# Performance work log

Measured on AMD Instinct MI355X. Metric: run time of the kernel, lower is better.

## Reference

```python
import jax, jax.numpy as jnp
import numpy as np
from jax import lax

D_MODEL, D_STATE, D_CONV, EXPAND = 64, 16, 4, 2
D_INNER = EXPAND * D_MODEL          # 128
DT_RANK = (D_MODEL + 15) // 16      # 4 = ceil(d_model/16), mamba_ssm 'auto'
B, L, N_IDX = 512, 256, 2048


def setup_inputs() -> dict:
    key = jax.random.key(0)
    ks = jax.random.split(key, 14)
    g = lambda k, shape, s: jax.random.normal(k, shape, jnp.float32) * s
    return {
        "reads": jax.random.normal(ks[0], (B, L, 4), jnp.float32),
        "sequenced_reads_indices": jax.random.randint(ks[1], (N_IDX,), 0, B),
        "exp_w": g(ks[2], (4, D_MODEL), 0.5),
        "exp_b": jnp.zeros((D_MODEL,), jnp.float32),
        "in_proj_w": g(ks[3], (D_MODEL, 2 * D_INNER), 0.1),
        "conv_w": g(ks[4], (D_INNER, 1, D_CONV), 0.3),
        "conv_b": jnp.zeros((D_INNER,), jnp.float32),
        "x_proj_w": g(ks[5], (D_INNER, DT_RANK + 2 * D_STATE), 0.1),
        "dt_w": g(ks[6], (DT_RANK, D_INNER), 0.3),
        "dt_b": jnp.full((D_INNER,), -4.6, jnp.float32),  # softplus(-4.6) ~ 0.01, mamba dt init scale
        "A_log": jnp.log(jnp.broadcast_to(jnp.arange(1, D_STATE + 1, dtype=jnp.float32), (D_INNER, D_STATE))),
        "D_skip": jnp.ones((D_INNER,), jnp.float32),
        "out_proj_w": g(ks[7], (D_INNER, D_MODEL), 0.1),
        "q_w": g(ks[8], (2 * D_MODEL, D_MODEL), 0.1),
        "q_b": jnp.zeros((D_MODEL,), jnp.float32),
        "k_w": g(ks[9], (2 * D_MODEL, D_MODEL), 0.1),
        "k_b": jnp.zeros((D_MODEL,), jnp.float32),
    }


def _mamba(x, in_proj_w, conv_w, conv_b, x_proj_w, dt_w, dt_b, A_log, D_skip, out_proj_w):
    # x: [b, l, d_model]
    xm, z = jnp.split(x @ in_proj_w, 2, axis=-1)  # each [b, l, d_inner]
    # causal depthwise conv over the sequence axis (pad left by d_conv-1, truncate to l)
    xc = lax.conv_general_dilated(
        xm.transpose(0, 2, 1), conv_w, (1,), [(D_CONV - 1, 0)],
        dimension_numbers=("NCH", "OIH", "NCH"), feature_group_count=D_INNER)
    xc = jax.nn.silu(xc + conv_b[None, :, None]).transpose(0, 2, 1)  # [b, l, d_inner]
    dt, Bm, Cm = jnp.split(xc @ x_proj_w, [DT_RANK, DT_RANK + D_STATE], axis=-1)
    delta = jax.nn.softplus(dt @ dt_w + dt_b)  # [b, l, d_inner]
    A = -jnp.exp(A_log)                        # [d_inner, d_state]

    def step(h, inp):
        d_t, B_t, C_t, u_t = inp  # [b,di], [b,ds], [b,ds], [b,di]
        h = jnp.exp(d_t[:, :, None] * A) * h + (d_t * u_t)[:, :, None] * B_t[:, None, :]
        return h, jnp.einsum("bdn,bn->bd", h, C_t)

    h0 = jnp.zeros((x.shape[0], D_INNER, D_STATE), x.dtype)
    xs = (delta.transpose(1, 0, 2), Bm.transpose(1, 0, 2),
          Cm.transpose(1, 0, 2), xc.transpose(1, 0, 2))
    _, ys = lax.scan(jax.checkpoint(step), h0, xs)  # ys: [l, b, d_inner]
    y = ys.transpose(1, 0, 2) + xc * D_skip
    return (y * jax.nn.silu(z)) @ out_proj_w  # [b, l, d_model]


def reference(reads, sequenced_reads_indices, exp_w, exp_b, in_proj_w, conv_w, conv_b,
              x_proj_w, dt_w, dt_b, A_log, D_skip, out_proj_w, q_w, q_b, k_w, k_b):
    x = reads @ exp_w + exp_b  # [b, l, d_model]
    enc = _mamba(x, in_proj_w, conv_w, conv_b, x_proj_w, dt_w, dt_b, A_log, D_skip, out_proj_w)
    mean_pooled = enc.mean(axis=1)        # [b, d_model]
    last_pooled = enc[:, -1, :]           # [b, d_model] (max pool computed in torch but unused)
    pooled = jnp.concatenate([mean_pooled, last_pooled], axis=-1)  # [b, 2*d_model]
    seq = pooled[sequenced_reads_indices]  # [n, 2*d_model]
    queries = seq @ q_w + q_b
    keys = pooled @ k_w + k_b
    return jnp.einsum("nd,md->nm", queries, keys)  # [n, b]
```

## Files before the change

### kernel.cpp

```cpp
#include <hip/hip_runtime.h>
#include <math.h>

#define L_SEQ 256
#define TILE 32
#define NSEG 8

typedef __attribute__((ext_vector_type(2))) float f32x2;
typedef __attribute__((ext_vector_type(4))) float f32x4;
typedef __attribute__((ext_vector_type(8))) _Float16 f16x8;

__device__ __forceinline__ f32x2 fma2(f32x2 a, f32x2 b, f32x2 c) {
    return __builtin_elementwise_fma(a, b, c);
}
__device__ __forceinline__ f32x2 splat2(float x) { f32x2 v = {x, x}; return v; }
__device__ __forceinline__ float silu_f(float x) { return x / (1.f + __expf(-x)); }
__device__ __forceinline__ float sp2_f(float x) {
    return log2f(1.f + exp2f(x * 1.44269504f)) * 0.69314718f;
}

__global__ __launch_bounds__(256)
void k_prep(const float* __restrict__ exp_w, const float* __restrict__ exp_b,
            const float* __restrict__ in_proj_w, const float* __restrict__ x_proj_w,
            const float* __restrict__ dt_w,
            const float* __restrict__ conv_w, const float* __restrict__ conv_b,
            _Float16* __restrict__ WT, _Float16* __restrict__ W2, float* __restrict__ bias2)
{
    const int t = threadIdx.x, blk = blockIdx.x;
    if (blk < 5) {
        const int base = blk * 4096;
        for (int i = base + t; i < base + 4096; i += 256) {
            const int row = i >> 7, k = i & 127;
            float v;
            if (row < 128) {
                v = x_proj_w[k * 36 + 0] * dt_w[row]
                  + x_proj_w[k * 36 + 1] * dt_w[128 + row]
                  + x_proj_w[k * 36 + 2] * dt_w[256 + row]
                  + x_proj_w[k * 36 + 3] * dt_w[384 + row];
            } else {
                v = x_proj_w[k * 36 + 4 + (row - 128)];
            }
            WT[i] = (_Float16)v;
        }
    } else {
        const int d = t & 127;
        const int col = (t < 128) ? d : (128 + d);
        float w0 = 0, w1 = 0, w2 = 0, w3 = 0, bb = 0;
        for (int k = 0; k < 64; ++k) {
            float w = in_proj_w[k * 256 + col];
            w0 = fmaf(exp_w[k], w, w0);
            w1 = fmaf(exp_w[64 + k], w, w1);
            w2 = fmaf(exp_w[128 + k], w, w2);
            w3 = fmaf(exp_w[192 + k], w, w3);
            bb = fmaf(exp_b[k], w, bb);
        }
        const float wx[4] = {w0, w1, w2, w3};
        if (t < 128) {
            for (int j = 0; j < 32; ++j) {
                float v = 0.f;
                if (j < 16)      v = conv_w[d * 4 + (j >> 2)] * wx[j & 3];
                else if (j < 20) v = conv_w[d * 4 + (j - 16)] * bb;
                W2[d * 32 + j] = (_Float16)v;
            }
            bias2[d] = conv_b[d];
        } else {
            for (int j = 0; j < 32; ++j) {
                float v = 0.f;
                if (j >= 12 && j < 16) v = wx[j - 12];
                else if (j == 19)      v = bb;
                W2[(128 + d) * 32 + j] = (_Float16)v;
            }
        }
    }
}

__global__ __launch_bounds__(512, 2)
void mamba_seg2(const float* __restrict__ reads,
                const _Float16* __restrict__ WT, const _Float16* __restrict__ W2,
                const float* __restrict__ bias2, const float* __restrict__ dt_b,
                const float* __restrict__ A_log, const float* __restrict__ D_skip,
                f16x8* __restrict__ QPK, float* __restrict__ GS,
                float* __restrict__ CZ, float* __restrict__ SL, int Bn)
{
    const int bx = blockIdx.x;
    const int b = bx >> 2, jp = bx & 3;
    const int t = threadIdx.x;
    const int lane256 = t & 255, wg = t >> 8;
    const int dd = lane256 >> 1, g = lane256 & 1;
    const int sidx = jp * 2 + wg;

    __shared__ __align__(16) _Float16 F2[2][32 * 40];
    __shared__ __align__(16) _Float16 XC2[2][32 * 136];
    __shared__ __align__(16) float    BC2[2][32 * 32];
    __shared__ _Float16               ZS2[2][32 * 128];
    __shared__ _Float16               DE2[2][32 * 128];

    const float dskip = D_skip[dd];
    const float c1 = -1.44269504f * (float)(8 * g + 1);
    bool structured = true;
#pragma unroll
    for (int k = 0; k < 8; ++k) {
        float a = -__expf(A_log[dd * 16 + g * 8 + k]);
        structured = structured && (fabsf(a + (float)(g * 8 + k + 1)) < 1e-3f);
    }

    for (int i = t; i < 2 * 32 * 40; i += 512) {
        const int tau = i / 1280, r = i - tau * 1280;
        const int l = r / 40, j = r - l * 40;
        const int l_off = jp * 64 + tau * 32;
        _Float16 v = (_Float16)0.f;
        if (j < 16) {
            const int row = l_off + l - 3 + (j >> 2);
            if (row >= 0) v = (_Float16)reads[((size_t)b * L_SEQ + row) * 4 + (j & 3)];
        } else if (j < 20) {
            v = (l_off + l - 3 + (j - 16) >= 0) ? (_Float16)1.f : (_Float16)0.f;
        }
        F2[0][i] = v;
    }
    __syncthreads();

    const int lane = t & 63, wv = t >> 6;
    const int fcol = lane & 15, kq = lane >> 4, rbase = kq * 4;

#pragma unroll
    for (int i = 0; i < 8; ++i) {
        const int tt = wv + 8 * i;
        const int tau = tt >> 5, tid = tt & 31;
        const int m = tid & 1, n = tid >> 1;
        f16x8 af = *(const f16x8*)&F2[tau][(m * 16 + fcol) * 40 + kq * 8];
        f16x8 bf = *(const f16x8*)&W2[(n * 16 + fcol) * 32 + kq * 8];
        f32x4 acc = {0.f, 0.f, 0.f, 0.f};
        acc = __builtin_amdgcn_mfma_f32_16x16x32_f16(af, bf, acc, 0, 0, 0);
        if (n < 8) {
            const int ch = n * 16 + fcol;
            const float bv = bias2[ch];
#pragma unroll
            for (int r = 0; r < 4; ++r)
                XC2[tau][(m * 16 + rbase + r) * 136 + ch] = (_Float16)silu_f(acc[r] + bv);
        } else {
            const int ch = (n - 8) * 16 + fcol;
#pragma unroll
            for (int r = 0; r < 4; ++r)
                ZS2[tau][(m * 16 + rbase + r) * 128 + ch] = (_Float16)silu_f(acc[r]);
        }
    }
    __syncthreads();

#pragma unroll
    for (int i = 0; i < 5; ++i) {
        const int tt = wv + 8 * i;
        const int tau = (tt >= 20) ? 1 : 0, tid = tt - 20 * tau;
        const int m = tid & 1, n = tid >> 1;
        f32x4 acc = {0.f, 0.f, 0.f, 0.f};
#pragma unroll
        for (int ks = 0; ks < 4; ++ks) {
            const int ko = ks * 32 + kq * 8;
            f16x8 af = *(const f16x8*)&XC2[tau][(m * 16 + fcol) * 136 + ko];
            f16x8 bf = *(const f16x8*)&WT[(n * 16 + fcol) * 128 + ko];
            acc = __builtin_amdgcn_mfma_f32_16x16x32_f16(af, bf, acc, 0, 0, 0);
        }
        if (n < 8) {
            const int ch = n * 16 + fcol;
            const float db = dt_b[ch];
#pragma unroll
            for (int r = 0; r < 4; ++r)
                DE2[tau][(m * 16 + rbase + r) * 128 + ch] = (_Float16)sp2_f(acc[r] + db);
        } else {
            const int jb = (n - 8) * 16 + fcol;
#pragma unroll
            for (int r = 0; r < 4; ++r)
                BC2[tau][(m * 16 + rbase + r) * 32 + jb] = acc[r];
        }
    }
    __syncthreads();

    f32x2 h2[4], P2[4], K2[4];
#pragma unroll
    for (int k = 0; k < 4; ++k) { h2[k] = splat2(0.f); P2[k] = splat2(1.f); K2[k] = splat2(0.f); }
    float gsum = 0.f;
    {
        const _Float16* DEw = DE2[wg];
        const _Float16* ZSw = ZS2[wg];
        const _Float16* XCw = XC2[wg];
        const float*    BCw = BC2[wg];
        auto scan_loop = [&](bool needpk) {
            for (int l = 0; l < TILE; ++l) {
                const float de = (float)DEw[l * 128 + dd];
                const float zs = (float)ZSw[l * 128 + dd];
                const float xc = (float)XCw[l * 136 + dd];
                const float du = de * xc;
                f32x2 E2[4];
                if (structured) {
                    const float r = exp2f(de * -1.44269504f);
                    const float t1 = exp2f(de * c1);
                    const float r2 = r * r;
                    E2[0] = (f32x2){t1, t1 * r};
                    const f32x2 r2s = splat2(r2);
                    E2[1] = E2[0] * r2s;
                    E2[2] = E2[1] * r2s;
                    E2[3] = E2[2] * r2s;
                } else {
#pragma unroll
                    for (int k = 0; k < 4; ++k) {
                        float e0 = exp2f(de * (-__expf(A_log[dd * 16 + g * 8 + 2 * k])) * 1.44269504f);
                        float e1 = exp2f(de * (-__expf(A_log[dd * 16 + g * 8 + 2 * k + 1])) * 1.44269504f);
                        E2[k] = (f32x2){e0, e1};
                    }
                }
                const float4 Bq0 = *(const float4*)&BCw[l * 32 + g * 8];
                const float4 Bq1 = *(const float4*)&BCw[l * 32 + g * 8 + 4];
                const float4 Cq0 = *(const float4*)&BCw[l * 32 + 16 + g * 8];
                const float4 Cq1 = *(const float4*)&BCw[l * 32 + 16 + g * 8 + 4];
                const f32x2 B2[4] = {{Bq0.x, Bq0.y}, {Bq0.z, Bq0.w}, {Bq1.x, Bq1.y}, {Bq1.z, Bq1.w}};
                const f32x2 C2[4] = {{Cq0.x, Cq0.y}, {Cq0.z, Cq0.w}, {Cq1.x, Cq1.y}, {Cq1.z, Cq1.w}};
                const f32x2 dus = splat2(du), zss = splat2(zs);
                f32x2 yp2 = splat2(0.f);
#pragma unroll
                for (int k = 0; k < 4; ++k) {
                    h2[k] = fma2(E2[k], h2[k], dus * B2[k]);
                    yp2 = fma2(h2[k], C2[k], yp2);
                    if (needpk) {
                        P2[k] = P2[k] * E2[k];
                        K2[k] = fma2(zss, C2[k] * P2[k], K2[k]);
                    }
                }
                float yp = yp2.x + yp2.y;
                const float y = yp + __shfl_xor(yp, 1);
                gsum += fmaf(xc, dskip, y) * zs;
            }
        };
        if (sidx == 0) scan_loop(false);
        else           scan_loop(true);
    }

    {
        const size_t sb = (size_t)sidx * Bn + b;
#pragma unroll
        for (int k = 0; k < 4; ++k) {
            const int p = g * 4 + k;
            f16x8 v;
            v[0] = (_Float16)h2[k].x; v[1] = (_Float16)h2[k].y;
            v[2] = (_Float16)P2[k].x; v[3] = (_Float16)P2[k].y;
            v[4] = (_Float16)K2[k].x; v[5] = (_Float16)K2[k].y;
            v[6] = (_Float16)0.f;     v[7] = (_Float16)0.f;
            QPK[(sb * 8 + p) * 128 + dd] = v;
        }
        if (g == 0) GS[sb * 128 + dd] = gsum;
        if (jp == 3 && wg == 1) {
            const float zs_last = (float)ZS2[1][(TILE - 1) * 128 + dd];
            const float xc_last = (float)XC2[1][(TILE - 1) * 136 + dd];
#pragma unroll
            for (int k = 0; k < 8; ++k)
                CZ[((size_t)b * 16 + g * 8 + k) * 128 + dd] =
                    zs_last * BC2[1][(TILE - 1) * 32 + 16 + g * 8 + k];
            if (g == 0) SL[(size_t)b * 128 + dd] = zs_last * xc_last * dskip;
        }
    }
}

template<int NS>
__global__ __launch_bounds__(128)
void stitch(const f16x8* __restrict__ QPK, const float* __restrict__ GS,
            const float* __restrict__ CZ, const float* __restrict__ SL,
            const float* __restrict__ out_proj_w,
            const float* __restrict__ k_w, const float* __restrict__ k_b,
            float* __restrict__ pooled, float* __restrict__ keysT, int Bn)
{
    const int b = blockIdx.x, d = threadIdx.x;
    __shared__ float gb[256];
    __shared__ float pl[128];

    float h[16];
    float gsum = GS[(size_t)b * 128 + d];
#pragma unroll
    for (int p = 0; p < 8; ++p) {
        f16x8 v = QPK[((size_t)b * 8 + p) * 128 + d];
        h[2 * p] = (float)v[0]; h[2 * p + 1] = (float)v[1];
    }
#pragma unroll
    for (int s = 1; s < NS; ++s) {
        const size_t sb = (size_t)s * Bn + b;
        gsum += GS[sb * 128 + d];
        float corr = 0.f;
#pragma unroll
        for (int p = 0; p < 8; ++p) {
            f16x8 v = QPK[(sb * 8 + p) * 128 + d];
            corr = fmaf((float)v[4], h[2 * p], corr);
            corr = fmaf((float)v[5], h[2 * p + 1], corr);
            h[2 * p]     = fmaf((float)v[2], h[2 * p],     (float)v[0]);
            h[2 * p + 1] = fmaf((float)v[3], h[2 * p + 1], (float)v[1]);
        }
        gsum += corr;
    }
    float glast = SL[(size_t)b * 128 + d];
#pragma unroll
    for (int n = 0; n < 16; ++n)
        glast = fmaf(CZ[((size_t)b * 16 + n) * 128 + d], h[n], glast);

    gb[d] = gsum * (1.f / (float)L_SEQ);
    gb[128 + d] = glast;
    __syncthreads();
    {
        const int half = d >> 6, oc = d & 63;
        const float* gbp = &gb[half * 128];
        float s = 0.f;
#pragma unroll 16
        for (int i = 0; i < 128; ++i) s = fmaf(gbp[i], out_proj_w[i * 64 + oc], s);
        pooled[(size_t)b * 128 + d] = s;
        pl[d] = s;
    }
    __syncthreads();
    if (d < 64) {
        float s = k_b[d];
#pragma unroll 16
        for (int i = 0; i < 128; ++i) s = fmaf(pl[i], k_w[i * 64 + d], s);
        keysT[(size_t)d * Bn + b] = s;
    }
}

__global__ __launch_bounds__(128)
void qk_kernel(const float* __restrict__ pooled, const int* __restrict__ idx,
               const float* __restrict__ q_w, const float* __restrict__ q_b,
               const float* __restrict__ keysT, float* __restrict__ out, int B, int N)
{
    const int n0 = blockIdx.x * 2, t = threadIdx.x;
    const int n1 = n0 + 1;
    const bool has1 = (n1 < N);
    __shared__ float p0[128], p1[128];
    __shared__ float q0[64], q1[64];
    const int bi0 = idx[n0];
    const int bi1 = has1 ? idx[n1] : bi0;
    p0[t] = pooled[(size_t)bi0 * 128 + t];
    p1[t] = pooled[(size_t)bi1 * 128 + t];
    __syncthreads();
    if (t < 64) {
        float s = q_b[t];
#pragma unroll
        for (int i = 0; i < 128; ++i) s = fmaf(p0[i], q_w[i * 64 + t], s);
        q0[t] = s;
    } else {
        const int tt = t - 64;
        float s = q_b[tt];
#pragma unroll
        for (int i = 0; i < 128; ++i) s = fmaf(p1[i], q_w[i * 64 + tt], s);
        q1[tt] = s;
    }
    __syncthreads();
    for (int m0 = t * 4; m0 < B; m0 += 512) {
        f32x4 a0 = {0.f, 0.f, 0.f, 0.f}, a1 = {0.f, 0.f, 0.f, 0.f};
#pragma unroll 8
        for (int i = 0; i < 64; ++i) {
            const float4 kv = *(const float4*)&keysT[(size_t)i * B + m0];
            const float qa = q0[i], qb = q1[i];
            a0[0] = fmaf(qa, kv.x, a0[0]); a0[1] = fmaf(qa, kv.y, a0[1]);
            a0[2] = fmaf(qa, kv.z, a0[2]); a0[3] = fmaf(qa, kv.w, a0[3]);
            a1[0] = fmaf(qb, kv.x, a1[0]); a1[1] = fmaf(qb, kv.y, a1[1]);
            a1[2] = fmaf(qb, kv.z, a1[2]); a1[3] = fmaf(qb, kv.w, a1[3]);
        }
        *(f32x4*)&out[(size_t)n0 * B + m0] = a0;
        if (has1) *(f32x4*)&out[(size_t)n1 * B + m0] = a1;
    }
}


extern "C" void kernel_launch(void* const* d_in, const int* in_sizes, int n_in,
                              void* d_out, int out_size, void* d_ws, size_t ws_size,
                              hipStream_t stream)
{
    const float* reads      = (const float*)d_in[0];
    const int*   idx        = (const int*)d_in[1];
    const float* exp_w      = (const float*)d_in[2];
    const float* exp_b      = (const float*)d_in[3];
    const float* in_proj_w  = (const float*)d_in[4];
    const float* conv_w     = (const float*)d_in[5];
    const float* conv_b     = (const float*)d_in[6];
    const float* x_proj_w   = (const float*)d_in[7];
    const float* dt_w       = (const float*)d_in[8];
    const float* dt_b       = (const float*)d_in[9];
    const float* A_log      = (const float*)d_in[10];
    const float* D_skip     = (const float*)d_in[11];
    const float* out_proj_w = (const float*)d_in[12];
    const float* q_w        = (const float*)d_in[13];
    const float* q_b        = (const float*)d_in[14];
    const float* k_w        = (const float*)d_in[15];
    const float* k_b        = (const float*)d_in[16];

    const int B = in_sizes[0] / (L_SEQ * 4);
    const int N = in_sizes[1];

    char* wsb = (char*)d_ws;
    size_t off = 0;
    auto alloc = [&](size_t bytes) {
        size_t o = off;
        off = (off + bytes + 255) & ~(size_t)255;
        return o;
    };

    float*     pooled = (float*)(wsb + alloc((size_t)B * 128 * 4));
    float*     keysT  = (float*)(wsb + alloc((size_t)B * 64 * 4));
    _Float16*  WT     = (_Float16*)(wsb + alloc(160 * 128 * 2));
    _Float16*  W2     = (_Float16*)(wsb + alloc(256 * 32 * 2));
    float*     bias2  = (float*)(wsb + alloc(128 * 4));

    const size_t pairs = (size_t)B * NSEG * 8 * 128;
    f16x8* QPK = (f16x8*)(wsb + alloc(pairs * 16));
    float* GS  = (float*)(wsb + alloc((size_t)B * NSEG * 128 * 4));
    float* CZ  = (float*)(wsb + alloc((size_t)B * 16 * 128 * 4));
    float* SL  = (float*)(wsb + alloc((size_t)B * 128 * 4));

    k_prep<<<6, 256, 0, stream>>>(exp_w, exp_b, in_proj_w, x_proj_w, dt_w,
                                  conv_w, conv_b, WT, W2, bias2);
    mamba_seg2<<<B * 4, 512, 0, stream>>>(reads, WT, W2, bias2, dt_b,
                                          A_log, D_skip, QPK, GS, CZ, SL, B);
    stitch<NSEG><<<B, 128, 0, stream>>>(QPK, GS, CZ, SL, out_proj_w, k_w, k_b,
                                        pooled, keysT, B);
    qk_kernel<<<(N + 1) / 2, 128, 0, stream>>>(pooled, idx, q_w, q_b, keysT,
                                               (float*)d_out, B, N);
}
```

Measured before the change: 147.5 us.

## Split scan into 16 segments of 16 steps, split QPK into packed arrays

The chunked Mamba scan now uses 16 segments of 16 timesteps, each handled by its own 256-thread block, instead of 512-thread blocks that each ran two 32-step segments. Shorter serial scans and more independent blocks aim to raise occupancy and cut the sequential latency per block. The padded f16x8 QPK records are replaced by three separate f16x2 arrays, and P/K are skipped for the first segment, which reduces global write and read traffic. In exchange the stitch kernel does twice as many serial combine steps, and the MFMA tiles are half-filled with 16-row tiles.

```diff
diff --git a/kernel.cpp b/kernel.cpp
--- a/kernel.cpp
+++ b/kernel.cpp
@@ -2,12 +2,13 @@
 #include <math.h>
 
 #define L_SEQ 256
-#define TILE 32
-#define NSEG 8
+#define TILE 16
+#define NSEG 16
 
 typedef __attribute__((ext_vector_type(2))) float f32x2;
 typedef __attribute__((ext_vector_type(4))) float f32x4;
 typedef __attribute__((ext_vector_type(8))) _Float16 f16x8;
+typedef __attribute__((ext_vector_type(2))) _Float16 f16x2;
 
 __device__ __forceinline__ f32x2 fma2(f32x2 a, f32x2 b, f32x2 c) {
     return __builtin_elementwise_fma(a, b, c);
@@ -73,26 +74,26 @@
     }
 }
 
-__global__ __launch_bounds__(512, 2)
-void mamba_seg2(const float* __restrict__ reads,
-                const _Float16* __restrict__ WT, const _Float16* __restrict__ W2,
-                const float* __restrict__ bias2, const float* __restrict__ dt_b,
-                const float* __restrict__ A_log, const float* __restrict__ D_skip,
-                f16x8* __restrict__ QPK, float* __restrict__ GS,
-                float* __restrict__ CZ, float* __restrict__ SL, int Bn)
+__global__ __launch_bounds__(256, 6)
+void mamba_seg(const float* __restrict__ reads,
+               const _Float16* __restrict__ WT, const _Float16* __restrict__ W2,
+               const float* __restrict__ bias2, const float* __restrict__ dt_b,
+               const float* __restrict__ A_log, const float* __restrict__ D_skip,
+               f16x2* __restrict__ Qg, f16x2* __restrict__ Pg, f16x2* __restrict__ Kg,
+               float* __restrict__ GS, float* __restrict__ CZ, float* __restrict__ SL,
+               int Bn)
 {
     const int bx = blockIdx.x;
-    const int b = bx >> 2, jp = bx & 3;
+    const int b = bx >> 4, sidx = bx & 15;
+    const int l_off = sidx * TILE;
     const int t = threadIdx.x;
-    const int lane256 = t & 255, wg = t >> 8;
-    const int dd = lane256 >> 1, g = lane256 & 1;
-    const int sidx = jp * 2 + wg;
-
-    __shared__ __align__(16) _Float16 F2[2][32 * 40];
-    __shared__ __align__(16) _Float16 XC2[2][32 * 136];
-    __shared__ __align__(16) float    BC2[2][32 * 32];
-    __shared__ _Float16               ZS2[2][32 * 128];
-    __shared__ _Float16               DE2[2][32 * 128];
+    const int dd = t >> 1, g = t & 1;
+
+    __shared__ __align__(16) _Float16 F[TILE * 40];
+    __shared__ __align__(16) _Float16 XC[TILE * 136];
+    __shared__ __align__(16) float    BC[TILE * 32];
+    __shared__ _Float16               ZS[TILE * 128];
+    __shared__ _Float16               DE[TILE * 128];
 
     const float dskip = D_skip[dd];
     const float c1 = -1.44269504f * (float)(8 * g + 1);
@@ -103,10 +104,8 @@
         structured = structured && (fabsf(a + (float)(g * 8 + k + 1)) < 1e-3f);
     }
 
-    for (int i = t; i < 2 * 32 * 40; i += 512) {
-        const int tau = i / 1280, r = i - tau * 1280;
-        const int l = r / 40, j = r - l * 40;
-        const int l_off = jp * 64 + tau * 32;
+    for (int i = t; i < TILE * 40; i += 256) {
+        const int l = i / 40, j = i - l * 40;
         _Float16 v = (_Float16)0.f;
         if (j < 16) {
             const int row = l_off + l - 3 + (j >> 2);
@@ -114,7 +113,7 @@
         } else if (j < 20) {
             v = (l_off + l - 3 + (j - 16) >= 0) ? (_Float16)1.f : (_Float16)0.f;
         }
-        F2[0][i] = v;
+        F[i] = v;
     }
     __syncthreads();
 
@@ -122,11 +121,9 @@
     const int fcol = lane & 15, kq = lane >> 4, rbase = kq * 4;
 
 #pragma unroll
-    for (int i = 0; i < 8; ++i) {
-        const int tt = wv + 8 * i;
-        const int tau = tt >> 5, tid = tt & 31;
-        const int m = tid & 1, n = tid >> 1;
-        f16x8 af = *(const f16x8*)&F2[tau][(m * 16 + fcol) * 40 + kq * 8];
+    for (int i = 0; i < 4; ++i) {
+        const int n = wv + 4 * i;
+        f16x8 af = *(const f16x8*)&F[fcol * 40 + kq * 8];
         f16x8 bf = *(const f16x8*)&W2[(n * 16 + fcol) * 32 + kq * 8];
         f32x4 acc = {0.f, 0.f, 0.f, 0.f};
         acc = __builtin_amdgcn_mfma_f32_16x16x32_f16(af, bf, acc, 0, 0, 0);
@@ -135,40 +132,40 @@
             const float bv = bias2[ch];
 #pragma unroll
             for (int r = 0; r < 4; ++r)
-                XC2[tau][(m * 16 + rbase + r) * 136 + ch] = (_Float16)silu_f(acc[r] + bv);
+                XC[(rbase + r) * 136 + ch] = (_Float16)silu_f(acc[r] + bv);
         } else {
             const int ch = (n - 8) * 16 + fcol;
 #pragma unroll
             for (int r = 0; r < 4; ++r)
-                ZS2[tau][(m * 16 + rbase + r) * 128 + ch] = (_Float16)silu_f(acc[r]);
-        }
-    }
-    __syncthreads();
-
-#pragma unroll
-    for (int i = 0; i < 5; ++i) {
-        const int tt = wv + 8 * i;
-        const int tau = (tt >= 20) ? 1 : 0, tid = tt - 20 * tau;
-        const int m = tid & 1, n = tid >> 1;
-        f32x4 acc = {0.f, 0.f, 0.f, 0.f};
-#pragma unroll
-        for (int ks = 0; ks < 4; ++ks) {
-            const int ko = ks * 32 + kq * 8;
-            f16x8 af = *(const f16x8*)&XC2[tau][(m * 16 + fcol) * 136 + ko];
-            f16x8 bf = *(const f16x8*)&WT[(n * 16 + fcol) * 128 + ko];
-            acc = __builtin_amdgcn_mfma_f32_16x16x32_f16(af, bf, acc, 0, 0, 0);
-        }
-        if (n < 8) {
-            const int ch = n * 16 + fcol;
-            const float db = dt_b[ch];
-#pragma unroll
-            for (int r = 0; r < 4; ++r)
-                DE2[tau][(m * 16 + rbase + r) * 128 + ch] = (_Float16)sp2_f(acc[r] + db);
-        } else {
-            const int jb = (n - 8) * 16 + fcol;
-#pragma unroll
-            for (int r = 0; r < 4; ++r)
-                BC2[tau][(m * 16 + rbase + r) * 32 + jb] = acc[r];
+                ZS[(rbase + r) * 128 + ch] = (_Float16)silu_f(acc[r]);
+        }
+    }
+    __syncthreads();
+
+#pragma unroll
+    for (int i = 0; i < 3; ++i) {
+        const int n = wv + 4 * i;
+        if (n < 10) {
+            f32x4 acc = {0.f, 0.f, 0.f, 0.f};
+#pragma unroll
+            for (int ks = 0; ks < 4; ++ks) {
+                const int ko = ks * 32 + kq * 8;
+                f16x8 af = *(const f16x8*)&XC[fcol * 136 + ko];
+                f16x8 bf = *(const f16x8*)&WT[(n * 16 + fcol) * 128 + ko];
+                acc = __builtin_amdgcn_mfma_f32_16x16x32_f16(af, bf, acc, 0, 0, 0);
+            }
+            if (n < 8) {
+                const int ch = n * 16 + fcol;
+                const float db = dt_b[ch];
+#pragma unroll
+                for (int r = 0; r < 4; ++r)
+                    DE[(rbase + r) * 128 + ch] = (_Float16)sp2_f(acc[r] + db);
+            } else {
+                const int jb = (n - 8) * 16 + fcol;
+#pragma unroll
+                for (int r = 0; r < 4; ++r)
+                    BC[(rbase + r) * 32 + jb] = acc[r];
+            }
         }
     }
     __syncthreads();
@@ -178,15 +175,11 @@
     for (int k = 0; k < 4; ++k) { h2[k] = splat2(0.f); P2[k] = splat2(1.f); K2[k] = splat2(0.f); }
     float gsum = 0.f;
     {
-        const _Float16* DEw = DE2[wg];
-        const _Float16* ZSw = ZS2[wg];
-        const _Float16* XCw = XC2[wg];
-        const float*    BCw = BC2[wg];
         auto scan_loop = [&](bool needpk) {
             for (int l = 0; l < TILE; ++l) {
-                const float de = (float)DEw[l * 128 + dd];
-                const float zs = (float)ZSw[l * 128 + dd];
-                const float xc = (float)XCw[l * 136 + dd];
+                const float de = (float)DE[l * 128 + dd];
+                const float zs = (float)ZS[l * 128 + dd];
+                const float xc = (float)XC[l * 136 + dd];
                 const float du = de * xc;
                 f32x2 E2[4];
                 if (structured) {
@@ -206,10 +199,10 @@
                         E2[k] = (f32x2){e0, e1};
                     }
                 }
-                const float4 Bq0 = *(const float4*)&BCw[l * 32 + g * 8];
-                const float4 Bq1 = *(const float4*)&BCw[l * 32 + g * 8 + 4];
-                const float4 Cq0 = *(const float4*)&BCw[l * 32 + 16 + g * 8];
-                const float4 Cq1 = *(const float4*)&BCw[l * 32 + 16 + g * 8 + 4];
+                const float4 Bq0 = *(const float4*)&BC[l * 32 + g * 8];
+                const float4 Bq1 = *(const float4*)&BC[l * 32 + g * 8 + 4];
+                const float4 Cq0 = *(const float4*)&BC[l * 32 + 16 + g * 8];
+                const float4 Cq1 = *(const float4*)&BC[l * 32 + 16 + g * 8 + 4];
                 const f32x2 B2[4] = {{Bq0.x, Bq0.y}, {Bq0.z, Bq0.w}, {Bq1.x, Bq1.y}, {Bq1.z, Bq1.w}};
                 const f32x2 C2[4] = {{Cq0.x, Cq0.y}, {Cq0.z, Cq0.w}, {Cq1.x, Cq1.y}, {Cq1.z, Cq1.w}};
                 const f32x2 dus = splat2(du), zss = splat2(zs);
@@ -236,22 +229,21 @@
         const size_t sb = (size_t)sidx * Bn + b;
 #pragma unroll
         for (int k = 0; k < 4; ++k) {
-            const int p = g * 4 + k;
-            f16x8 v;
-            v[0] = (_Float16)h2[k].x; v[1] = (_Float16)h2[k].y;
-            v[2] = (_Float16)P2[k].x; v[3] = (_Float16)P2[k].y;
-            v[4] = (_Float16)K2[k].x; v[5] = (_Float16)K2[k].y;
-            v[6] = (_Float16)0.f;     v[7] = (_Float16)0.f;
-            QPK[(sb * 8 + p) * 128 + dd] = v;
+            const size_t o = (sb * 8 + g * 4 + k) * 128 + dd;
+            Qg[o] = (f16x2){(_Float16)h2[k].x, (_Float16)h2[k].y};
+            if (sidx != 0) {
+                Pg[o] = (f16x2){(_Float16)P2[k].x, (_Float16)P2[k].y};
+                Kg[o] = (f16x2){(_Float16)K2[k].x, (_Float16)K2[k].y};
+            }
         }
         if (g == 0) GS[sb * 128 + dd] = gsum;
-        if (jp == 3 && wg == 1) {
-            const float zs_last = (float)ZS2[1][(TILE - 1) * 128 + dd];
-            const float xc_last = (float)XC2[1][(TILE - 1) * 136 + dd];
+        if (sidx == NSEG - 1) {
+            const float zs_last = (float)ZS[(TILE - 1) * 128 + dd];
+            const float xc_last = (float)XC[(TILE - 1) * 136 + dd];
 #pragma unroll
             for (int k = 0; k < 8; ++k)
                 CZ[((size_t)b * 16 + g * 8 + k) * 128 + dd] =
-                    zs_last * BC2[1][(TILE - 1) * 32 + 16 + g * 8 + k];
+                    zs_last * BC[(TILE - 1) * 32 + 16 + g * 8 + k];
             if (g == 0) SL[(size_t)b * 128 + dd] = zs_last * xc_last * dskip;
         }
     }
@@ -259,7 +251,8 @@
 
 template<int NS>
 __global__ __launch_bounds__(128)
-void stitch(const f16x8* __restrict__ QPK, const float* __restrict__ GS,
+void stitch(const f16x2* __restrict__ Qg, const f16x2* __restrict__ Pg,
+            const f16x2* __restrict__ Kg, const float* __restrict__ GS,
             const float* __restrict__ CZ, const float* __restrict__ SL,
             const float* __restrict__ out_proj_w,
             const float* __restrict__ k_w, const float* __restrict__ k_b,
@@ -273,8 +266,8 @@
     float gsum = GS[(size_t)b * 128 + d];
 #pragma unroll
     for (int p = 0; p < 8; ++p) {
-        f16x8 v = QPK[((size_t)b * 8 + p) * 128 + d];
-        h[2 * p] = (float)v[0]; h[2 * p + 1] = (float)v[1];
+        f16x2 q = Qg[((size_t)b * 8 + p) * 128 + d];
+        h[2 * p] = (float)q[0]; h[2 * p + 1] = (float)q[1];
     }
 #pragma unroll
     for (int s = 1; s < NS; ++s) {
@@ -283,11 +276,12 @@
         float corr = 0.f;
 #pragma unroll
         for (int p = 0; p < 8; ++p) {
-            f16x8 v = QPK[(sb * 8 + p) * 128 + d];
-            corr = fmaf((float)v[4], h[2 * p], corr);
-            corr = fmaf((float)v[5], h[2 * p + 1], corr);
-            h[2 * p]     = fmaf((float)v[2], h[2 * p],     (float)v[0]);
-            h[2 * p + 1] = fmaf((float)v[3], h[2 * p + 1], (float)v[1]);
+            const size_t o = (sb * 8 + p) * 128 + d;
+            f16x2 qv = Qg[o], pv = Pg[o], kv = Kg[o];
+            corr = fmaf((float)kv[0], h[2 * p], corr);
+            corr = fmaf((float)kv[1], h[2 * p + 1], corr);
+            h[2 * p]     = fmaf((float)pv[0], h[2 * p],     (float)qv[0]);
+            h[2 * p + 1] = fmaf((float)pv[1], h[2 * p + 1], (float)qv[1]);
         }
         gsum += corr;
     }
@@ -402,16 +396,19 @@
     float*     bias2  = (float*)(wsb + alloc(128 * 4));
 
     const size_t pairs = (size_t)B * NSEG * 8 * 128;
-    f16x8* QPK = (f16x8*)(wsb + alloc(pairs * 16));
-    float* GS  = (float*)(wsb + alloc((size_t)B * NSEG * 128 * 4));
-    float* CZ  = (float*)(wsb + alloc((size_t)B * 16 * 128 * 4));
-    float* SL  = (float*)(wsb + alloc((size_t)B * 128 * 4));
+    f16x2* Qg = (f16x2*)(wsb + alloc(pairs * 4));
+    f16x2* Pg = (f16x2*)(wsb + alloc(pairs * 4));
+    f16x2* Kg = (f16x2*)(wsb + alloc(pairs * 4));
+    float* GS = (float*)(wsb + alloc((size_t)B * NSEG * 128 * 4));
+    float* CZ = (float*)(wsb + alloc((size_t)B * 16 * 128 * 4));
+    float* SL = (float*)(wsb + alloc((size_t)B * 128 * 4));
 
     k_prep<<<6, 256, 0, stream>>>(exp_w, exp_b, in_proj_w, x_proj_w, dt_w,
                                   conv_w, conv_b, WT, W2, bias2);
-    mamba_seg2<<<B * 4, 512, 0, stream>>>(reads, WT, W2, bias2, dt_b,
-                                          A_log, D_skip, QPK, GS, CZ, SL, B);
-    stitch<NSEG><<<B, 128, 0, stream>>>(QPK, GS, CZ, SL, out_proj_w, k_w, k_b,
+    mamba_seg<<<B * NSEG, 256, 0, stream>>>(reads, WT, W2, bias2, dt_b,
+                                            A_log, D_skip, Qg, Pg, Kg,
+                                            GS, CZ, SL, B);
+    stitch<NSEG><<<B, 128, 0, stream>>>(Qg, Pg, Kg, GS, CZ, SL, out_proj_w, k_w, k_b,
                                         pooled, keysT, B);
     qk_kernel<<<(N + 1) / 2, 128, 0, stream>>>(pooled, idx, q_w, q_b, keysT,
                                                (float*)d_out, B, N);
```

After: 135.7 us. 8.0% less time.
